# Optimization experiments

Measured on AMD Instinct MI355X. Metric: run time of the kernel, lower is better.

Reference implementation:

```python
import jax, jax.numpy as jnp
import numpy as np

VOCAB, EMB, HID = 32000, 512, 1024

def setup_inputs() -> dict:
    key = jax.random.key(0)
    k1, k2, k3, k4, k5, k6 = jax.random.split(key, 6)
    s_e = 1.0 / np.sqrt(EMB)
    s_h = 1.0 / np.sqrt(HID)
    return {
        "x": jax.random.randint(k1, (32, 512), 0, VOCAB, dtype=jnp.int64),
        "emb_table": jax.random.normal(k2, (VOCAB, EMB), dtype=jnp.float32),
        "W_ih": jax.random.uniform(k3, (4 * HID, EMB), jnp.float32, -s_h, s_h),
        "W_hh": jax.random.uniform(k4, (4 * HID, HID), jnp.float32, -s_h, s_h),
        "b_ih": jax.random.uniform(k5, (4 * HID,), jnp.float32, -s_h, s_h),
        "b_hh": jax.random.uniform(k6, (4 * HID,), jnp.float32, -s_h, s_h),
    }

def _lstm(embedded, W_ih, W_hh, b_ih, b_hh):
    # embedded: [B, T, E]; gates order (PyTorch): i, f, g, o
    B = embedded.shape[0]
    H = W_hh.shape[1]
    # Precompute input projections for all timesteps: [B, T, 4H]
    x_proj = jnp.einsum('bte,ge->btg', embedded, W_ih) + b_ih + b_hh

    def step(carry, xt):
        h, c = carry
        gates = xt + h @ W_hh.T  # [B, 4H]
        i, f, g, o = jnp.split(gates, 4, axis=-1)
        i = jax.nn.sigmoid(i)
        f = jax.nn.sigmoid(f)
        g = jnp.tanh(g)
        o = jax.nn.sigmoid(o)
        c = f * c + i * g
        h = o * jnp.tanh(c)
        return (h, c), h

    h0 = jnp.zeros((B, H), embedded.dtype)
    c0 = jnp.zeros((B, H), embedded.dtype)
    (h_f, c_f), hs = jax.lax.scan(step, (h0, c0), jnp.swapaxes(x_proj, 0, 1))
    return jnp.swapaxes(hs, 0, 1), h_f, c_f

def reference(x, emb_table, W_ih, W_hh, b_ih, b_hh):
    embedded = emb_table[x]  # [B, T, E]
    encoder_outputs, state_h, state_c = _lstm(embedded, W_ih, W_hh, b_ih, b_hh)
    return encoder_outputs, state_h, state_c
```

## Files before the change

kernel.cpp:

```cpp
#include <hip/hip_runtime.h>

#define Bb 32
#define Tt 512
#define Ee 512
#define Hh 1024

typedef __attribute__((ext_vector_type(8))) short bf16x8;
typedef __attribute__((ext_vector_type(4))) float f32x4;
typedef __attribute__((ext_vector_type(4))) unsigned u32x4;
typedef unsigned long long u64;

#define SEN 0x7FC0u

__device__ __forceinline__ unsigned short f2bf(float f) {
  unsigned int u = __float_as_uint(f);
  u = (u + 0x7fffu + ((u >> 16) & 1u)) >> 16;
  return (unsigned short)u;
}
__device__ __forceinline__ float sigmoidf_(float x) {
  x = fminf(fmaxf(x, -30.f), 30.f);
  return 1.f / (1.f + __expf(-x));
}
__device__ __forceinline__ float tanh_fast(float x) {
  float xx = fminf(fmaxf(x, -15.f), 15.f);
  float e = __expf(2.f * xx);
  return (e - 1.f) / (e + 1.f);
}
__device__ __forceinline__ bool frag_bad(u32x4 v) {
  return ((v[0] & 0xFFFFu) == SEN) | ((v[1] & 0xFFFFu) == SEN) |
         ((v[2] & 0xFFFFu) == SEN) | ((v[3] & 0xFFFFu) == SEN);
}

__global__ void gather_kernel(const int* __restrict__ x,
                              const float* __restrict__ emb,
                              unsigned short* __restrict__ emb_hi,
                              unsigned short* __restrict__ hbuf) {
  long long gid = (long long)blockIdx.x * blockDim.x + threadIdx.x;
  long long stride = (long long)gridDim.x * blockDim.x;
  for (long long i = gid; i < 8192; i += stride)
    ((ushort4*)hbuf)[i] = make_ushort4(0, 0, 0, 0);
  for (long long i = 8192 + gid; i < 4194304; i += stride)
    ((ushort4*)hbuf)[i] =
        make_ushort4((unsigned short)SEN, (unsigned short)SEN,
                     (unsigned short)SEN, (unsigned short)SEN);
  long long n4 = (long long)Bb * Tt * Ee / 4;
  for (long long i = gid; i < n4; i += stride) {
    long long bt = i >> 7;
    int e4 = (int)(i & 127);
    int row = x[bt];
    row = min(max(row, 0), 31999);
    float4 v = ((const float4*)(emb + (long long)row * Ee))[e4];
    ushort4 hv;
    hv.x = f2bf(v.x); hv.y = f2bf(v.y);
    hv.z = f2bf(v.z); hv.w = f2bf(v.w);
    ((ushort4*)emb_hi)[i] = hv;
  }
}

__global__ __launch_bounds__(256, 1)
void lstm_kernel(const unsigned short* __restrict__ emb_hi,
                 unsigned short* __restrict__ hbuf,
                 const float* __restrict__ W_ih,
                 const float* __restrict__ W_hh,
                 const float* __restrict__ b_ih,
                 const float* __restrict__ b_hh,
                 float* __restrict__ out) {
  __shared__ unsigned short sWih[32 * 512];
  __shared__ unsigned short sWhh[32 * 1024];
  __shared__ float sAcc[2][2][2][2][16][17];
  __shared__ float sBias[32];
  __shared__ float sC[32][8];

  const int tid = threadIdx.x;
  const int lane = tid & 63;
  const int wv = tid >> 6;
  const int wg = blockIdx.x;
  const int j0 = (wg & 7) * 128 + (wg >> 3) * 8;

  for (int idx = tid; idx < 32 * 64; idx += 256) {
    int c = idx >> 6, k8 = idx & 63;
    int grow = (c >> 3) * Hh + j0 + (c & 7);
    const float* src = W_ih + (long long)grow * Ee + k8 * 8;
    int us = (c * 512 + k8 * 8) ^ ((c & 7) << 3);
#pragma unroll
    for (int j = 0; j < 8; j++) sWih[us + j] = f2bf(src[j]);
  }
  for (int idx = tid; idx < 32 * 128; idx += 256) {
    int c = idx >> 7, k8 = idx & 127;
    int grow = (c >> 3) * Hh + j0 + (c & 7);
    const float* src = W_hh + (long long)grow * Hh + k8 * 8;
    int us = (c * 1024 + k8 * 8) ^ ((c & 7) << 3);
#pragma unroll
    for (int j = 0; j < 8; j++) sWhh[us + j] = f2bf(src[j]);
  }
  if (tid < 32) {
    int grow = (tid >> 3) * Hh + j0 + (tid & 7);
    sBias[tid] = b_ih[grow] + b_hh[grow];
  }
  sC[tid >> 3][tid & 7] = 0.f;
  __syncthreads();

  const int r16 = lane & 15;
  const int kg = (lane >> 4) * 8;
  const int col = lane & 15;
  const int kw = wv & 1;
  const int mt = wv >> 1;
  const int rb = mt * 16 + r16;

  float h_last = 0.f, c_last = 0.f;

  for (int t = 0; t < Tt; t++) {
    __builtin_amdgcn_sched_barrier(0);

    const u32x4* hb4 = (const u32x4*)(hbuf + (u64)t * 32768);
    const u64* hb8 = (const u64*)(hbuf + (u64)t * 32768);
    u32x4 hA[16];
    int iA[16];
#pragma unroll
    for (int q = 0; q < 16; q++) {
      int kc = q * 2 + kw;
      iA[q] = (rb * Hh + kc * 32 + kg) >> 3;
      hA[q] = hb4[iA[q]];
    }

    f32x4 acc[2];
    acc[0] = (f32x4){0.f, 0.f, 0.f, 0.f};
    acc[1] = (f32x4){0.f, 0.f, 0.f, 0.f};
#pragma unroll
    for (int q = 0; q < 8; q++) {
      int kc = q * 2 + kw;
      int ai = (rb * Tt + t) * Ee + kc * 32 + kg;
      bf16x8 aH = *(const bf16x8*)(emb_hi + ai);
#pragma unroll
      for (int bt = 0; bt < 2; bt++) {
        int c = bt * 16 + col;
        int bo = (c * 512 + kc * 32 + kg) ^ ((c & 7) << 3);
        bf16x8 bW = *(const bf16x8*)(sWih + bo);
        acc[bt] = __builtin_amdgcn_mfma_f32_16x16x32_bf16(aH, bW, acc[bt], 0, 0, 0);
      }
    }

#pragma unroll
    for (int q = 0; q < 16; q++) {
      int kc = q * 2 + kw;
      u32x4 va = hA[q];
      bool bad = frag_bad(va);
      while (__any(bad)) {
        if (bad) {
          u64 a0 = __hip_atomic_load(hb8 + iA[q] * 2, __ATOMIC_RELAXED,
                                     __HIP_MEMORY_SCOPE_AGENT);
          u64 a1 = __hip_atomic_load(hb8 + iA[q] * 2 + 1, __ATOMIC_RELAXED,
                                     __HIP_MEMORY_SCOPE_AGENT);
          va[0] = (unsigned)a0; va[1] = (unsigned)(a0 >> 32);
          va[2] = (unsigned)a1; va[3] = (unsigned)(a1 >> 32);
        }
        bad = frag_bad(va);
      }
      union { u32x4 u; bf16x8 v; } ua;
      ua.u = va;
#pragma unroll
      for (int bt = 0; bt < 2; bt++) {
        int c = bt * 16 + col;
        int bo = (c * 1024 + kc * 32 + kg) ^ ((c & 7) << 3);
        bf16x8 bW = *(const bf16x8*)(sWhh + bo);
        acc[bt] = __builtin_amdgcn_mfma_f32_16x16x32_bf16(ua.v, bW, acc[bt], 0, 0, 0);
      }
    }

#pragma unroll
    for (int bt = 0; bt < 2; bt++)
#pragma unroll
      for (int r = 0; r < 4; r++)
        sAcc[t & 1][kw][mt][bt][(lane >> 4) * 4 + r][col] = acc[bt][r];
    __syncthreads();

    {
      int b = tid >> 3, u = tid & 7;
      int mtc = b >> 4, rr = b & 15;
      float g0 = sAcc[t & 1][0][mtc][0][rr][u] +
                 sAcc[t & 1][1][mtc][0][rr][u] + sBias[u];
      float g1 = sAcc[t & 1][0][mtc][0][rr][8 + u] +
                 sAcc[t & 1][1][mtc][0][rr][8 + u] + sBias[8 + u];
      float g2 = sAcc[t & 1][0][mtc][1][rr][u] +
                 sAcc[t & 1][1][mtc][1][rr][u] + sBias[16 + u];
      float g3 = sAcc[t & 1][0][mtc][1][rr][8 + u] +
                 sAcc[t & 1][1][mtc][1][rr][8 + u] + sBias[24 + u];
      float ig = sigmoidf_(g0);
      float fg = sigmoidf_(g1);
      float gg = tanh_fast(g2);
      float og = sigmoidf_(g3);
      float cn = fg * sC[b][u] + ig * gg;
      sC[b][u] = cn;
      float hn = og * tanh_fast(cn);
      h_last = hn; c_last = cn;

      unsigned pack = (unsigned)f2bf(hn);
      unsigned other = __shfl_xor(pack, 1, 64);
      if (t + 1 < Tt && (u & 1) == 0) {
        unsigned w = (pack & 0xffffu) | (other << 16);
        unsigned* nb32 = (unsigned*)(hbuf + (u64)(t + 1) * 32768);
        __hip_atomic_store(nb32 + ((b * 1024 + j0 + u) >> 1), w,
                           __ATOMIC_RELAXED, __HIP_MEMORY_SCOPE_AGENT);
      }
      out[((long long)b * Tt + t) * Hh + j0 + u] = hn;
    }
  }

  {
    int b = tid >> 3, u = tid & 7;
    int hj = j0 + u;
    out[16777216LL + b * Hh + hj] = h_last;
    out[16777216LL + 32768 + b * Hh + hj] = c_last;
  }
}

extern "C" void kernel_launch(void* const* d_in, const int* in_sizes, int n_in,
                              void* d_out, int out_size, void* d_ws, size_t ws_size,
                              hipStream_t stream) {
  const int* x      = (const int*)d_in[0];
  const float* emb  = (const float*)d_in[1];
  const float* W_ih = (const float*)d_in[2];
  const float* W_hh = (const float*)d_in[3];
  const float* b_ih = (const float*)d_in[4];
  const float* b_hh = (const float*)d_in[5];
  float* out = (float*)d_out;

  unsigned short* emb_hi = (unsigned short*)d_ws;
  unsigned short* hbuf   = emb_hi + 8388608;

  hipLaunchKernelGGL(gather_kernel, dim3(2048), dim3(256), 0, stream,
                     x, emb, emb_hi, hbuf);

  void* args[] = { (void*)&emb_hi, (void*)&hbuf,
                   (void*)&W_ih, (void*)&W_hh, (void*)&b_ih, (void*)&b_hh,
                   (void*)&out };
  hipError_t e = hipLaunchCooperativeKernel((void*)lstm_kernel, dim3(128),
                                            dim3(256), args, 0, stream);
  if (e != hipSuccess) {
    hipLaunchKernelGGL(lstm_kernel, dim3(128), dim3(256), 0, stream,
                       emb_hi, hbuf, W_ih, W_hh, b_ih, b_hh, out);
  }
}
```

Baseline: 2.856 ms.

## Halve LSTM workgroups to 64, widen hidden slice, stream W_ih from global

```diff
diff --git a/kernel.cpp b/kernel.cpp
--- a/kernel.cpp
+++ b/kernel.cpp
@@ -34,7 +34,9 @@
 __global__ void gather_kernel(const int* __restrict__ x,
                               const float* __restrict__ emb,
                               unsigned short* __restrict__ emb_hi,
-                              unsigned short* __restrict__ hbuf) {
+                              unsigned short* __restrict__ hbuf,
+                              unsigned short* __restrict__ wih_bf,
+                              int wih_flag) {
   long long gid = (long long)blockIdx.x * blockDim.x + threadIdx.x;
   long long stride = (long long)gridDim.x * blockDim.x;
   for (long long i = gid; i < 8192; i += stride)
@@ -55,49 +57,60 @@
     hv.z = f2bf(v.z); hv.w = f2bf(v.w);
     ((ushort4*)emb_hi)[i] = hv;
   }
-}
-
+  if (wih_flag) {
+  }
+}
+
+__global__ void wconv_kernel(const float* __restrict__ W_ih,
+                             unsigned short* __restrict__ wih_bf) {
+  long long gid = (long long)blockIdx.x * blockDim.x + threadIdx.x;
+  long long stride = (long long)gridDim.x * blockDim.x;
+  for (long long i = gid; i < 524288; i += stride) {
+    float4 v = ((const float4*)W_ih)[i];
+    ushort4 hv;
+    hv.x = f2bf(v.x); hv.y = f2bf(v.y);
+    hv.z = f2bf(v.z); hv.w = f2bf(v.w);
+    ((ushort4*)wih_bf)[i] = hv;
+  }
+}
+
+template <bool PRE>
 __global__ __launch_bounds__(256, 1)
 void lstm_kernel(const unsigned short* __restrict__ emb_hi,
                  unsigned short* __restrict__ hbuf,
+                 const unsigned short* __restrict__ wih_bf,
                  const float* __restrict__ W_ih,
                  const float* __restrict__ W_hh,
                  const float* __restrict__ b_ih,
                  const float* __restrict__ b_hh,
                  float* __restrict__ out) {
-  __shared__ unsigned short sWih[32 * 512];
-  __shared__ unsigned short sWhh[32 * 1024];
-  __shared__ float sAcc[2][2][2][2][16][17];
-  __shared__ float sBias[32];
-  __shared__ float sC[32][8];
+  __shared__ unsigned short sWhh[64 * 1024];
+  __shared__ float sAcc[2][2][4][16][17];
 
   const int tid = threadIdx.x;
   const int lane = tid & 63;
   const int wv = tid >> 6;
   const int wg = blockIdx.x;
-  const int j0 = (wg & 7) * 128 + (wg >> 3) * 8;
-
-  for (int idx = tid; idx < 32 * 64; idx += 256) {
-    int c = idx >> 6, k8 = idx & 63;
-    int grow = (c >> 3) * Hh + j0 + (c & 7);
-    const float* src = W_ih + (long long)grow * Ee + k8 * 8;
-    int us = (c * 512 + k8 * 8) ^ ((c & 7) << 3);
-#pragma unroll
-    for (int j = 0; j < 8; j++) sWih[us + j] = f2bf(src[j]);
-  }
-  for (int idx = tid; idx < 32 * 128; idx += 256) {
+  const int j0 = (wg & 7) * 128 + (wg >> 3) * 16;
+
+  for (int idx = tid; idx < 64 * 128; idx += 256) {
     int c = idx >> 7, k8 = idx & 127;
-    int grow = (c >> 3) * Hh + j0 + (c & 7);
+    int grow = (c >> 4) * Hh + j0 + (c & 15);
     const float* src = W_hh + (long long)grow * Hh + k8 * 8;
     int us = (c * 1024 + k8 * 8) ^ ((c & 7) << 3);
 #pragma unroll
     for (int j = 0; j < 8; j++) sWhh[us + j] = f2bf(src[j]);
   }
-  if (tid < 32) {
-    int grow = (tid >> 3) * Hh + j0 + (tid & 7);
-    sBias[tid] = b_ih[grow] + b_hh[grow];
-  }
-  sC[tid >> 3][tid & 7] = 0.f;
+
+  const int bb = tid >> 3, uu = tid & 7;
+  float bias[4][2];
+#pragma unroll
+  for (int g = 0; g < 4; g++) {
+    bias[g][0] = b_ih[g * Hh + j0 + uu] + b_hh[g * Hh + j0 + uu];
+    bias[g][1] = b_ih[g * Hh + j0 + 8 + uu] + b_hh[g * Hh + j0 + 8 + uu];
+  }
+  float c0 = 0.f, c1 = 0.f;
+  float hL0 = 0.f, hL1 = 0.f, cL0 = 0.f, cL1 = 0.f;
   __syncthreads();
 
   const int r16 = lane & 15;
@@ -107,8 +120,6 @@
   const int mt = wv >> 1;
   const int rb = mt * 16 + r16;
 
-  float h_last = 0.f, c_last = 0.f;
-
   for (int t = 0; t < Tt; t++) {
     __builtin_amdgcn_sched_barrier(0);
 
@@ -123,20 +134,34 @@
       hA[q] = hb4[iA[q]];
     }
 
-    f32x4 acc[2];
-    acc[0] = (f32x4){0.f, 0.f, 0.f, 0.f};
-    acc[1] = (f32x4){0.f, 0.f, 0.f, 0.f};
+    f32x4 acc[4];
+#pragma unroll
+    for (int g = 0; g < 4; g++) acc[g] = (f32x4){0.f, 0.f, 0.f, 0.f};
 #pragma unroll
     for (int q = 0; q < 8; q++) {
       int kc = q * 2 + kw;
       int ai = (rb * Tt + t) * Ee + kc * 32 + kg;
       bf16x8 aH = *(const bf16x8*)(emb_hi + ai);
 #pragma unroll
-      for (int bt = 0; bt < 2; bt++) {
-        int c = bt * 16 + col;
-        int bo = (c * 512 + kc * 32 + kg) ^ ((c & 7) << 3);
-        bf16x8 bW = *(const bf16x8*)(sWih + bo);
-        acc[bt] = __builtin_amdgcn_mfma_f32_16x16x32_bf16(aH, bW, acc[bt], 0, 0, 0);
+      for (int g = 0; g < 4; g++) {
+        long long grow = (long long)(g * Hh + j0 + col);
+        bf16x8 bW;
+        if constexpr (PRE) {
+          bW = *(const bf16x8*)(wih_bf + grow * Ee + kc * 32 + kg);
+        } else {
+          const float* wp = W_ih + grow * Ee + kc * 32 + kg;
+          float4 w0 = *(const float4*)wp;
+          float4 w1 = *(const float4*)(wp + 4);
+          unsigned p0, p1, p2, p3;
+          asm("v_cvt_pk_bf16_f32 %0, %1, %2" : "=v"(p0) : "v"(w0.x), "v"(w0.y));
+          asm("v_cvt_pk_bf16_f32 %0, %1, %2" : "=v"(p1) : "v"(w0.z), "v"(w0.w));
+          asm("v_cvt_pk_bf16_f32 %0, %1, %2" : "=v"(p2) : "v"(w1.x), "v"(w1.y));
+          asm("v_cvt_pk_bf16_f32 %0, %1, %2" : "=v"(p3) : "v"(w1.z), "v"(w1.w));
+          union { unsigned u[4]; bf16x8 v; } uw;
+          uw.u[0] = p0; uw.u[1] = p1; uw.u[2] = p2; uw.u[3] = p3;
+          bW = uw.v;
+        }
+        acc[g] = __builtin_amdgcn_mfma_f32_16x16x32_bf16(aH, bW, acc[g], 0, 0, 0);
       }
     }
 
@@ -159,59 +184,58 @@
       union { u32x4 u; bf16x8 v; } ua;
       ua.u = va;
 #pragma unroll
-      for (int bt = 0; bt < 2; bt++) {
-        int c = bt * 16 + col;
+      for (int g = 0; g < 4; g++) {
+        int c = g * 16 + col;
         int bo = (c * 1024 + kc * 32 + kg) ^ ((c & 7) << 3);
         bf16x8 bW = *(const bf16x8*)(sWhh + bo);
-        acc[bt] = __builtin_amdgcn_mfma_f32_16x16x32_bf16(ua.v, bW, acc[bt], 0, 0, 0);
-      }
-    }
-
-#pragma unroll
-    for (int bt = 0; bt < 2; bt++)
+        acc[g] = __builtin_amdgcn_mfma_f32_16x16x32_bf16(ua.v, bW, acc[g], 0, 0, 0);
+      }
+    }
+
+#pragma unroll
+    for (int g = 0; g < 4; g++)
 #pragma unroll
       for (int r = 0; r < 4; r++)
-        sAcc[t & 1][kw][mt][bt][(lane >> 4) * 4 + r][col] = acc[bt][r];
+        sAcc[kw][mt][g][(lane >> 4) * 4 + r][col] = acc[g][r];
     __syncthreads();
 
     {
-      int b = tid >> 3, u = tid & 7;
-      int mtc = b >> 4, rr = b & 15;
-      float g0 = sAcc[t & 1][0][mtc][0][rr][u] +
-                 sAcc[t & 1][1][mtc][0][rr][u] + sBias[u];
-      float g1 = sAcc[t & 1][0][mtc][0][rr][8 + u] +
-                 sAcc[t & 1][1][mtc][0][rr][8 + u] + sBias[8 + u];
-      float g2 = sAcc[t & 1][0][mtc][1][rr][u] +
-                 sAcc[t & 1][1][mtc][1][rr][u] + sBias[16 + u];
-      float g3 = sAcc[t & 1][0][mtc][1][rr][8 + u] +
-                 sAcc[t & 1][1][mtc][1][rr][8 + u] + sBias[24 + u];
-      float ig = sigmoidf_(g0);
-      float fg = sigmoidf_(g1);
-      float gg = tanh_fast(g2);
-      float og = sigmoidf_(g3);
-      float cn = fg * sC[b][u] + ig * gg;
-      sC[b][u] = cn;
-      float hn = og * tanh_fast(cn);
-      h_last = hn; c_last = cn;
-
-      unsigned pack = (unsigned)f2bf(hn);
-      unsigned other = __shfl_xor(pack, 1, 64);
-      if (t + 1 < Tt && (u & 1) == 0) {
-        unsigned w = (pack & 0xffffu) | (other << 16);
-        unsigned* nb32 = (unsigned*)(hbuf + (u64)(t + 1) * 32768);
-        __hip_atomic_store(nb32 + ((b * 1024 + j0 + u) >> 1), w,
-                           __ATOMIC_RELAXED, __HIP_MEMORY_SCOPE_AGENT);
-      }
-      out[((long long)b * Tt + t) * Hh + j0 + u] = hn;
-    }
-  }
-
-  {
-    int b = tid >> 3, u = tid & 7;
-    int hj = j0 + u;
-    out[16777216LL + b * Hh + hj] = h_last;
-    out[16777216LL + 32768 + b * Hh + hj] = c_last;
-  }
+      int mtc = bb >> 4, rr = bb & 15;
+#pragma unroll
+      for (int half = 0; half < 2; half++) {
+        int ui = uu + half * 8;
+        float g0 = sAcc[0][mtc][0][rr][ui] + sAcc[1][mtc][0][rr][ui] + bias[0][half];
+        float g1 = sAcc[0][mtc][1][rr][ui] + sAcc[1][mtc][1][rr][ui] + bias[1][half];
+        float g2 = sAcc[0][mtc][2][rr][ui] + sAcc[1][mtc][2][rr][ui] + bias[2][half];
+        float g3 = sAcc[0][mtc][3][rr][ui] + sAcc[1][mtc][3][rr][ui] + bias[3][half];
+        float ig = sigmoidf_(g0);
+        float fg = sigmoidf_(g1);
+        float gg = tanh_fast(g2);
+        float og = sigmoidf_(g3);
+        float cp = half ? c1 : c0;
+        float cn = fg * cp + ig * gg;
+        if (half) c1 = cn; else c0 = cn;
+        float hn = og * tanh_fast(cn);
+        if (half) { hL1 = hn; cL1 = cn; } else { hL0 = hn; cL0 = cn; }
+
+        unsigned pack = (unsigned)f2bf(hn);
+        unsigned other = __shfl_xor(pack, 1, 64);
+        if (t + 1 < Tt && (uu & 1) == 0) {
+          unsigned w = (pack & 0xffffu) | (other << 16);
+          unsigned* nb32 = (unsigned*)(hbuf + (u64)(t + 1) * 32768);
+          __hip_atomic_store(nb32 + ((bb * Hh + j0 + ui) >> 1), w,
+                             __ATOMIC_RELAXED, __HIP_MEMORY_SCOPE_AGENT);
+        }
+        out[((long long)bb * Tt + t) * Hh + j0 + ui] = hn;
+      }
+    }
+    __syncthreads();
+  }
+
+  out[16777216LL + bb * Hh + j0 + uu] = hL0;
+  out[16777216LL + bb * Hh + j0 + 8 + uu] = hL1;
+  out[16777216LL + 32768 + bb * Hh + j0 + uu] = cL0;
+  out[16777216LL + 32768 + bb * Hh + j0 + 8 + uu] = cL1;
 }
 
 extern "C" void kernel_launch(void* const* d_in, const int* in_sizes, int n_in,
@@ -227,17 +251,29 @@
 
   unsigned short* emb_hi = (unsigned short*)d_ws;
   unsigned short* hbuf   = emb_hi + 8388608;
+  unsigned short* wih_bf = hbuf + 16777216;
+
+  bool pre = (ws_size >= 54525952ull);
 
   hipLaunchKernelGGL(gather_kernel, dim3(2048), dim3(256), 0, stream,
-                     x, emb, emb_hi, hbuf);
-
-  void* args[] = { (void*)&emb_hi, (void*)&hbuf,
-                   (void*)&W_ih, (void*)&W_hh, (void*)&b_ih, (void*)&b_hh,
-                   (void*)&out };
-  hipError_t e = hipLaunchCooperativeKernel((void*)lstm_kernel, dim3(128),
-                                            dim3(256), args, 0, stream);
-  if (e != hipSuccess) {
-    hipLaunchKernelGGL(lstm_kernel, dim3(128), dim3(256), 0, stream,
-                       emb_hi, hbuf, W_ih, W_hh, b_ih, b_hh, out);
-  }
-}
+                     x, emb, emb_hi, hbuf, wih_bf, 0);
+  if (pre)
+    hipLaunchKernelGGL(wconv_kernel, dim3(512), dim3(256), 0, stream,
+                       W_ih, wih_bf);
+
+  void* args[] = { (void*)&emb_hi, (void*)&hbuf, (void*)&wih_bf, (void*)&W_ih,
+                   (void*)&W_hh, (void*)&b_ih, (void*)&b_hh, (void*)&out };
+  if (pre) {
+    hipError_t e = hipLaunchCooperativeKernel((void*)lstm_kernel<true>,
+                                              dim3(64), dim3(256), args, 0, stream);
+    if (e != hipSuccess)
+      hipLaunchKernelGGL(lstm_kernel<true>, dim3(64), dim3(256), 0, stream,
+                         emb_hi, hbuf, wih_bf, W_ih, W_hh, b_ih, b_hh, out);
+  } else {
+    hipError_t e = hipLaunchCooperativeKernel((void*)lstm_kernel<false>,
+                                              dim3(64), dim3(256), args, 0, stream);
+    if (e != hipSuccess)
+      hipLaunchKernelGGL(lstm_kernel<false>, dim3(64), dim3(256), 0, stream,
+                         emb_hi, hbuf, wih_bf, W_ih, W_hh, b_ih, b_hh, out);
+  }
+}
```

After: 3.406 ms. +19.3%, slower.
